# Optimization experiments

Hardware: AMD Instinct MI355X
Metric: run time of the kernel (lower is better)

The kernel has to match this reference:

```python
import jax, jax.numpy as jnp
import numpy as np

N0, N1, N2 = 200000, 50000, 10000   # node counts per hop (src -> layer1 targets -> layer2 targets)
E1, E2 = 1000000, 250000
C_IN, H = 128, 256


def setup_inputs() -> dict:
    key = jax.random.key(0)
    ks = jax.random.split(key, 10)
    return {
        "x": jax.random.normal(ks[0], (N0, C_IN), dtype=jnp.float32),
        "src1": jax.random.randint(ks[1], (E1,), 0, N0, dtype=jnp.int32),
        "dst1": jax.random.randint(ks[2], (E1,), 0, N1, dtype=jnp.int32),
        "src2": jax.random.randint(ks[3], (E2,), 0, N1, dtype=jnp.int32),
        "dst2": jax.random.randint(ks[4], (E2,), 0, N2, dtype=jnp.int32),
        "Wl1": jax.random.normal(ks[5], (C_IN, H), dtype=jnp.float32) / np.sqrt(C_IN),
        "Wr1": jax.random.normal(ks[6], (C_IN, H), dtype=jnp.float32) / np.sqrt(C_IN),
        "b1": jnp.zeros((H,), dtype=jnp.float32),
        "Wl2": jax.random.normal(ks[7], (H, H), dtype=jnp.float32) / np.sqrt(H),
        "Wr2": jax.random.normal(ks[8], (H, H), dtype=jnp.float32) / np.sqrt(H),
        "b2": jnp.zeros((H,), dtype=jnp.float32),
    }


def _sage_conv(x_src, x_dst, src, dst, Wl, Wr, b, n_dst):
    # mean aggregation of neighbor messages (PyG SAGEConv, aggr='mean', root_weight=True)
    msgs = x_src[src]                                             # [E, C] irregular gather
    agg = jax.ops.segment_sum(msgs, dst, num_segments=n_dst)      # [n_dst, C]
    cnt = jax.ops.segment_sum(jnp.ones_like(dst, dtype=x_src.dtype), dst, num_segments=n_dst)
    agg = agg / jnp.maximum(cnt, 1.0)[:, None]
    return agg @ Wl + x_dst @ Wr + b


def reference(x, src1, dst1, src2, dst2, Wl1, Wr1, b1, Wl2, Wr2, b2):
    # layer 1: targets are first N1 nodes
    h = _sage_conv(x, x[:N1], src1, dst1, Wl1, Wr1, b1, N1)       # [N1, H]
    h = jax.nn.relu(h)                                            # dropout: eval mode (identity)
    # layer 2: targets are first N2 nodes of the layer-1 output
    out = _sage_conv(h, h[:N2], src2, dst2, Wl2, Wr2, b2, N2)     # [N2, H]
    return out
```

## Files before the change

### kernel.cpp

```cpp
#include <hip/hip_runtime.h>

#define N0 200000
#define N1 50000
#define N2 10000
#define E1 1000000
#define E2 250000
#define CIN 128
#define HD  256

#define SH1   7
#define PK1   18
#define NB1   391
#define CAP1  3072
#define DPB1  128
#define SH2   6
#define PK2   16
#define NB2   157
#define CAP2  2048
#define DPB2  64

#define NBIN1 489
#define NBIN2 123
#define NPREP 768
#define NCVT  25000

typedef __attribute__((ext_vector_type(8))) short short8;
typedef __attribute__((ext_vector_type(4))) float f32x4;

__device__ __forceinline__ unsigned short f2bf(float f) {
    unsigned u = __builtin_bit_cast(unsigned, f);
    u = (u + 0x7fffu + ((u >> 16) & 1u)) >> 16;
    return (unsigned short)u;
}
__device__ __forceinline__ float bf2f(unsigned short h) {
    unsigned u = ((unsigned)h) << 16;
    return __builtin_bit_cast(float, u);
}

template<int SHIFTB, int PACKSH, int CAP>
__device__ __forceinline__ void bin_body(
    int bb, const int* __restrict__ src, const int* __restrict__ dst,
    int* __restrict__ gcnt, unsigned* __restrict__ binned, int E, int* sh)
{
    int* hcnt  = sh;
    int* hbase = sh + 512;
    int* hcur  = sh + 1024;
    const int t = threadIdx.x;
    hcnt[t] = 0; hcnt[t + 256] = 0;
    __syncthreads();

    unsigned pk[8];
    int      bk[8];
    const int e0 = bb * 2048;
    #pragma unroll
    for (int j = 0; j < 8; j++) {
        const int e = e0 + j * 256 + t;
        if (e < E) {
            const int d = dst[e];
            const int s = src[e];
            bk[j] = d >> SHIFTB;
            pk[j] = ((unsigned)(d & ((1 << SHIFTB) - 1)) << PACKSH) | (unsigned)s;
            atomicAdd(&hcnt[bk[j]], 1);
        } else bk[j] = -1;
    }
    __syncthreads();

    hbase[t]       = atomicAdd(&gcnt[t], hcnt[t]);             hcur[t] = 0;
    hbase[t + 256] = atomicAdd(&gcnt[t + 256], hcnt[t + 256]); hcur[t + 256] = 0;
    __syncthreads();

    #pragma unroll
    for (int j = 0; j < 8; j++) {
        if (bk[j] >= 0) {
            const int idx = atomicAdd(&hcur[bk[j]], 1);
            binned[(size_t)bk[j] * CAP + hbase[bk[j]] + idx] = pk[j];
        }
    }
}

__global__ __launch_bounds__(256) void megaA_kernel(
    const float* __restrict__ x, unsigned short* __restrict__ xb,
    const float* __restrict__ Wl1, const float* __restrict__ Wr1,
    const float* __restrict__ Wl2, const float* __restrict__ Wr2,
    unsigned short* __restrict__ wsw1, unsigned short* __restrict__ wsw2,
    const int* __restrict__ src1, const int* __restrict__ dst1,
    const int* __restrict__ src2, const int* __restrict__ dst2,
    int* __restrict__ gcnt1, int* __restrict__ gcnt2,
    unsigned* __restrict__ binned1, unsigned* __restrict__ binned2)
{
    __shared__ int sh[1536];
    const int b = blockIdx.x;
    const int t = threadIdx.x;

    if (b < NBIN1) {
        bin_body<SH1, PK1, CAP1>(b, src1, dst1, gcnt1, binned1, E1, sh);
    } else if (b < NBIN1 + NBIN2) {
        bin_body<SH2, PK2, CAP2>(b - NBIN1, src2, dst2, gcnt2, binned2, E2, sh);
    } else if (b < NBIN1 + NBIN2 + NPREP) {
        const int pb = b - NBIN1 - NBIN2;
        const float* Wl; const float* Wr; unsigned short* wsw; int K, tid;
        if (pb < 256) { Wl = Wl1; Wr = Wr1; wsw = wsw1; K = CIN; tid = pb * 256 + t; }
        else          { Wl = Wl2; Wr = Wr2; wsw = wsw2; K = HD;  tid = (pb - 256) * 256 + t; }
        const int j  = tid & 7;
        const int L  = (tid >> 3) & 63;
        const int nt = (tid >> 9) & 15;
        const int kt = tid >> 13;
        const int k  = kt * 32 + (L >> 4) * 8 + j;
        const int n  = nt * 16 + (L & 15);
        const float v = (k < K) ? Wl[(size_t)k * HD + n]
                                : Wr[(size_t)(k - K) * HD + n];
        wsw[tid] = f2bf(v);
    } else {
        const int i = (b - NBIN1 - NBIN2 - NPREP) * 256 + t;
        const float4 v = ((const float4*)x)[i];
        ushort4 o;
        o.x = f2bf(v.x); o.y = f2bf(v.y); o.z = f2bf(v.z); o.w = f2bf(v.w);
        ((ushort4*)xb)[i] = o;
    }
}

__global__ __launch_bounds__(512) void layer1_mega(
    const unsigned short* __restrict__ xb,
    const unsigned* __restrict__ binned1, const int* __restrict__ gcnt1,
    const unsigned short* __restrict__ wsw1, const float* __restrict__ bias,
    unsigned short* __restrict__ hb)
{
    __shared__ int ebuf[CAP1];
    __shared__ int lhist[DPB1], loff[DPB1], lcur[DPB1];
    __shared__ __align__(16) unsigned short aggT[4 * 128 * 4 * 8];

    const int t = threadIdx.x;
    const int b = blockIdx.x;
    const int cnt = gcnt1[b];
    const unsigned* bp = binned1 + (size_t)b * CAP1;

    if (t < DPB1) lhist[t] = 0;
    __syncthreads();
    for (int i = t; i < cnt; i += 512)
        atomicAdd(&lhist[bp[i] >> PK1], 1);
    __syncthreads();
    const int h0 = (t < DPB1) ? lhist[t] : 0;
    __syncthreads();
    #pragma unroll
    for (int ofs = 1; ofs < DPB1; ofs <<= 1) {
        const int u = (t >= ofs && t < DPB1) ? lhist[t - ofs] : 0;
        __syncthreads();
        if (t < DPB1) lhist[t] += u;
        __syncthreads();
    }
    if (t < DPB1) { loff[t] = lhist[t] - h0; lcur[t] = lhist[t] - h0; }
    __syncthreads();
    for (int i = t; i < cnt; i += 512) {
        const unsigned p = bp[i];
        const int slot = atomicAdd(&lcur[p >> PK1], 1);
        ebuf[slot] = (int)(p & ((1u << PK1) - 1u));
    }
    __syncthreads();

    const int w = t >> 6, L = t & 63, half = L >> 5, l32 = L & 31;
    const int ktw = l32 >> 3, qw = (l32 >> 1) & 3, jo = (l32 & 1) * 4;
    for (int r = w; r < DPB1; r += 8) {
        const int rg = b * DPB1 + r;
        if (rg < N1) {
            const int base = loff[r];
            const int n    = lcur[r] - loff[r];
            float ax = 0.f, ay = 0.f, az = 0.f, aw = 0.f;
            int i = half;
            for (; i + 6 < n; i += 8) {
                const int s0 = ebuf[base + i];
                const int s1 = ebuf[base + i + 2];
                const int s2 = ebuf[base + i + 4];
                const int s3 = ebuf[base + i + 6];
                const ushort4 v0 = *(const ushort4*)(xb + (size_t)s0 * CIN + l32 * 4);
                const ushort4 v1 = *(const ushort4*)(xb + (size_t)s1 * CIN + l32 * 4);
                const ushort4 v2 = *(const ushort4*)(xb + (size_t)s2 * CIN + l32 * 4);
                const ushort4 v3 = *(const ushort4*)(xb + (size_t)s3 * CIN + l32 * 4);
                ax += bf2f(v0.x) + bf2f(v1.x) + bf2f(v2.x) + bf2f(v3.x);
                ay += bf2f(v0.y) + bf2f(v1.y) + bf2f(v2.y) + bf2f(v3.y);
                az += bf2f(v0.z) + bf2f(v1.z) + bf2f(v2.z) + bf2f(v3.z);
                aw += bf2f(v0.w) + bf2f(v1.w) + bf2f(v2.w) + bf2f(v3.w);
            }
            for (; i < n; i += 2) {
                const int s = ebuf[base + i];
                const ushort4 v = *(const ushort4*)(xb + (size_t)s * CIN + l32 * 4);
                ax += bf2f(v.x); ay += bf2f(v.y); az += bf2f(v.z); aw += bf2f(v.w);
            }
            ax += __shfl_xor(ax, 32);
            ay += __shfl_xor(ay, 32);
            az += __shfl_xor(az, 32);
            aw += __shfl_xor(aw, 32);
            if (half == 0) {
                const float s = 1.0f / fmaxf((float)n, 1.0f);
                ushort4 o;
                o.x = f2bf(ax * s); o.y = f2bf(ay * s);
                o.z = f2bf(az * s); o.w = f2bf(aw * s);
                *(ushort4*)&aggT[(((ktw * 128 + r) * 4 + qw) * 8) + jo] = o;
            }
        }
    }
    __syncthreads();

    const int m = L & 15, q = L >> 4;
    const int row_l = w * 16 + m;
    const int rg2 = min(b * DPB1 + row_l, N1 - 1);
    const unsigned short* a2p = xb + (size_t)rg2 * CIN + q * 8;

    f32x4 acc[16];
    #pragma unroll
    for (int nt = 0; nt < 16; nt++) acc[nt] = (f32x4){0.f, 0.f, 0.f, 0.f};

    #pragma unroll
    for (int kt = 0; kt < 8; kt++) {
        short8 af;
        if (kt < 4) af = *(const short8*)&aggT[((kt * 128 + row_l) * 4 + q) * 8];
        else        af = *(const short8*)(a2p + (kt - 4) * 32);
        #pragma unroll
        for (int nt = 0; nt < 16; nt++) {
            const short8 bf = *(const short8*)(
                wsw1 + (((size_t)kt * 16 + nt) * 64 + L) * 8);
            acc[nt] = __builtin_amdgcn_mfma_f32_16x16x32_bf16(af, bf, acc[nt], 0, 0, 0);
        }
    }

    const int orow0 = b * DPB1 + w * 16 + q * 4;
    #pragma unroll
    for (int nt = 0; nt < 16; nt++) {
        const int col = nt * 16 + m;
        const float bv = bias[col];
        #pragma unroll
        for (int r = 0; r < 4; r++) {
            const int row = orow0 + r;
            if (row < N1) {
                const float v = fmaxf(acc[nt][r] + bv, 0.0f);
                hb[(size_t)row * HD + col] = f2bf(v);
            }
        }
    }
}

__global__ __launch_bounds__(512) void layer2_mega(
    const unsigned short* __restrict__ hb,
    const unsigned* __restrict__ binned2, const int* __restrict__ gcnt2,
    const unsigned short* __restrict__ wsw2, const float* __restrict__ bias,
    float* __restrict__ outp)
{
    __shared__ int ebuf[CAP2];
    __shared__ int lhist[DPB2], loff[DPB2], lcur[DPB2];
    __shared__ __align__(16) unsigned short aggT[8 * 64 * 4 * 8];

    const int t = threadIdx.x;
    const int b = blockIdx.x;
    const int cnt = gcnt2[b];
    const unsigned* bp = binned2 + (size_t)b * CAP2;

    if (t < DPB2) lhist[t] = 0;
    __syncthreads();
    for (int i = t; i < cnt; i += 512)
        atomicAdd(&lhist[bp[i] >> PK2], 1);
    __syncthreads();
    const int h0 = (t < DPB2) ? lhist[t] : 0;
    __syncthreads();
    #pragma unroll
    for (int ofs = 1; ofs < DPB2; ofs <<= 1) {
        const int u = (t >= ofs && t < DPB2) ? lhist[t - ofs] : 0;
        __syncthreads();
        if (t < DPB2) lhist[t] += u;
        __syncthreads();
    }
    if (t < DPB2) { loff[t] = lhist[t] - h0; lcur[t] = lhist[t] - h0; }
    __syncthreads();
    for (int i = t; i < cnt; i += 512) {
        const unsigned p = bp[i];
        const int slot = atomicAdd(&lcur[p >> PK2], 1);
        ebuf[slot] = (int)(p & ((1u << PK2) - 1u));
    }
    __syncthreads();

    const int w = t >> 6, L = t & 63;
    const int kt2 = L >> 3, q2 = (L >> 1) & 3, jo2 = (L & 1) * 4;
    for (int r = w; r < DPB2; r += 8) {
        const int rg = b * DPB2 + r;
        if (rg < N2) {
            const int base = loff[r];
            const int n    = lcur[r] - loff[r];
            float ax = 0.f, ay = 0.f, az = 0.f, aw = 0.f;
            int i = 0;
            for (; i + 3 < n; i += 4) {
                const int s0 = ebuf[base + i];
                const int s1 = ebuf[base + i + 1];
                const int s2 = ebuf[base + i + 2];
                const int s3 = ebuf[base + i + 3];
                const ushort4 v0 = *(const ushort4*)(hb + (size_t)s0 * HD + L * 4);
                const ushort4 v1 = *(const ushort4*)(hb + (size_t)s1 * HD + L * 4);
                const ushort4 v2 = *(const ushort4*)(hb + (size_t)s2 * HD + L * 4);
                const ushort4 v3 = *(const ushort4*)(hb + (size_t)s3 * HD + L * 4);
                ax += bf2f(v0.x) + bf2f(v1.x) + bf2f(v2.x) + bf2f(v3.x);
                ay += bf2f(v0.y) + bf2f(v1.y) + bf2f(v2.y) + bf2f(v3.y);
                az += bf2f(v0.z) + bf2f(v1.z) + bf2f(v2.z) + bf2f(v3.z);
                aw += bf2f(v0.w) + bf2f(v1.w) + bf2f(v2.w) + bf2f(v3.w);
            }
            for (; i < n; i++) {
                const int s = ebuf[base + i];
                const ushort4 v = *(const ushort4*)(hb + (size_t)s * HD + L * 4);
                ax += bf2f(v.x); ay += bf2f(v.y); az += bf2f(v.z); aw += bf2f(v.w);
            }
            const float s = 1.0f / fmaxf((float)n, 1.0f);
            ushort4 o;
            o.x = f2bf(ax * s); o.y = f2bf(ay * s);
            o.z = f2bf(az * s); o.w = f2bf(aw * s);
            *(ushort4*)&aggT[(((kt2 * 64 + r) * 4 + q2) * 8) + jo2] = o;
        }
    }
    __syncthreads();

    const int m = L & 15, q = L >> 4;
    const int mt = w & 3, nh = w >> 2;
    const int row_l = mt * 16 + m;
    const int rg2 = min(b * DPB2 + row_l, N2 - 1);
    const unsigned short* a2p = hb + (size_t)rg2 * HD + q * 8;

    f32x4 acc[8];
    #pragma unroll
    for (int nt = 0; nt < 8; nt++) acc[nt] = (f32x4){0.f, 0.f, 0.f, 0.f};

    #pragma unroll
    for (int kt = 0; kt < 16; kt++) {
        short8 af;
        if (kt < 8) af = *(const short8*)&aggT[((kt * 64 + row_l) * 4 + q) * 8];
        else        af = *(const short8*)(a2p + (kt - 8) * 32);
        #pragma unroll
        for (int nt = 0; nt < 8; nt++) {
            const short8 bf = *(const short8*)(
                wsw2 + (((size_t)kt * 16 + (nh * 8 + nt)) * 64 + L) * 8);
            acc[nt] = __builtin_amdgcn_mfma_f32_16x16x32_bf16(af, bf, acc[nt], 0, 0, 0);
        }
    }

    const int orow0 = b * DPB2 + mt * 16 + q * 4;
    #pragma unroll
    for (int nt = 0; nt < 8; nt++) {
        const int col = (nh * 8 + nt) * 16 + m;
        const float bv = bias[col];
        #pragma unroll
        for (int r = 0; r < 4; r++) {
            const int row = orow0 + r;
            if (row < N2)
                outp[(size_t)row * HD + col] = acc[nt][r] + bv;
        }
    }
}

extern "C" void kernel_launch(void* const* d_in, const int* in_sizes, int n_in,
                              void* d_out, int out_size, void* d_ws, size_t ws_size,
                              hipStream_t stream)
{
    const float* x    = (const float*)d_in[0];
    const int*   src1 = (const int*)  d_in[1];
    const int*   dst1 = (const int*)  d_in[2];
    const int*   src2 = (const int*)  d_in[3];
    const int*   dst2 = (const int*)  d_in[4];
    const float* Wl1  = (const float*)d_in[5];
    const float* Wr1  = (const float*)d_in[6];
    const float* b1   = (const float*)d_in[7];
    const float* Wl2  = (const float*)d_in[8];
    const float* Wr2  = (const float*)d_in[9];
    const float* b2   = (const float*)d_in[10];
    float* out = (float*)d_out;

    unsigned short* xb   = (unsigned short*)d_ws;
    unsigned short* hb   = xb + (size_t)N0 * CIN;
    unsigned short* wsw1 = hb + (size_t)N1 * HD;
    unsigned short* wsw2 = wsw1 + 2 * CIN * HD;
    int* gcnt1 = (int*)(wsw2 + 2 * HD * HD);
    int* gcnt2 = gcnt1 + 512;
    unsigned* binned1 = (unsigned*)(gcnt2 + 512);
    unsigned* binned2 = binned1 + (size_t)NB1 * CAP1;

    hipMemsetAsync(gcnt1, 0, 1024 * sizeof(int), stream);

    megaA_kernel<<<NBIN1 + NBIN2 + NPREP + NCVT, 256, 0, stream>>>(
        x, xb, Wl1, Wr1, Wl2, Wr2, wsw1, wsw2,
        src1, dst1, src2, dst2, gcnt1, gcnt2, binned1, binned2);

    layer1_mega<<<NB1, 512, 0, stream>>>(xb, binned1, gcnt1, wsw1, b1, hb);
    layer2_mega<<<NB2, 512, 0, stream>>>(hb, binned2, gcnt2, wsw2, b2, out);
}
```

Before: 310.2 us.

## Shrink destination bins to double layer1 and quadruple layer2 block counts

Halves the destinations per block in layer 1 (128 to 64) and cuts layer 2 from 64 to 16, so the launches have 782 and 625 blocks instead of 391 and 157 and can fill more compute units. The binning histograms grow to 1024 buckets, and the MFMA output tiling is re-split across warps so each warp covers fewer columns. The gather loops are also unrolled to issue 8 independent loads before accumulating, to hide more memory latency. The smaller per-bin capacities (2048 and 640 edges) leave less headroom for skewed degree distributions, and each block now reloads its full weight slice, which adds weight traffic.

Result: no change. 306.8 us (-1.1%).

```diff
diff --git a/kernel.cpp b/kernel.cpp
--- a/kernel.cpp
+++ b/kernel.cpp
@@ -8,16 +8,16 @@
 #define CIN 128
 #define HD  256
 
-#define SH1   7
+#define SH1   6
 #define PK1   18
-#define NB1   391
-#define CAP1  3072
-#define DPB1  128
-#define SH2   6
+#define NB1   782
+#define CAP1  2048
+#define DPB1  64
+#define SH2   4
 #define PK2   16
-#define NB2   157
-#define CAP2  2048
-#define DPB2  64
+#define NB2   625
+#define CAP2  640
+#define DPB2  16
 
 #define NBIN1 489
 #define NBIN2 123
@@ -43,10 +43,11 @@
     int* __restrict__ gcnt, unsigned* __restrict__ binned, int E, int* sh)
 {
     int* hcnt  = sh;
-    int* hbase = sh + 512;
-    int* hcur  = sh + 1024;
+    int* hbase = sh + 1024;
+    int* hcur  = sh + 2048;
     const int t = threadIdx.x;
-    hcnt[t] = 0; hcnt[t + 256] = 0;
+    #pragma unroll
+    for (int j = 0; j < 4; j++) hcnt[t + j * 256] = 0;
     __syncthreads();
 
     unsigned pk[8];
@@ -65,8 +66,12 @@
     }
     __syncthreads();
 
-    hbase[t]       = atomicAdd(&gcnt[t], hcnt[t]);             hcur[t] = 0;
-    hbase[t + 256] = atomicAdd(&gcnt[t + 256], hcnt[t + 256]); hcur[t + 256] = 0;
+    #pragma unroll
+    for (int j = 0; j < 4; j++) {
+        const int i = t + j * 256;
+        hbase[i] = atomicAdd(&gcnt[i], hcnt[i]);
+        hcur[i]  = 0;
+    }
     __syncthreads();
 
     #pragma unroll
@@ -88,7 +93,7 @@
     int* __restrict__ gcnt1, int* __restrict__ gcnt2,
     unsigned* __restrict__ binned1, unsigned* __restrict__ binned2)
 {
-    __shared__ int sh[1536];
+    __shared__ int sh[3072];
     const int b = blockIdx.x;
     const int t = threadIdx.x;
 
@@ -127,7 +132,7 @@
 {
     __shared__ int ebuf[CAP1];
     __shared__ int lhist[DPB1], loff[DPB1], lcur[DPB1];
-    __shared__ __align__(16) unsigned short aggT[4 * 128 * 4 * 8];
+    __shared__ __align__(16) unsigned short aggT[4 * DPB1 * 4 * 8];
 
     const int t = threadIdx.x;
     const int b = blockIdx.x;
@@ -166,19 +171,18 @@
             const int n    = lcur[r] - loff[r];
             float ax = 0.f, ay = 0.f, az = 0.f, aw = 0.f;
             int i = half;
-            for (; i + 6 < n; i += 8) {
-                const int s0 = ebuf[base + i];
-                const int s1 = ebuf[base + i + 2];
-                const int s2 = ebuf[base + i + 4];
-                const int s3 = ebuf[base + i + 6];
-                const ushort4 v0 = *(const ushort4*)(xb + (size_t)s0 * CIN + l32 * 4);
-                const ushort4 v1 = *(const ushort4*)(xb + (size_t)s1 * CIN + l32 * 4);
-                const ushort4 v2 = *(const ushort4*)(xb + (size_t)s2 * CIN + l32 * 4);
-                const ushort4 v3 = *(const ushort4*)(xb + (size_t)s3 * CIN + l32 * 4);
-                ax += bf2f(v0.x) + bf2f(v1.x) + bf2f(v2.x) + bf2f(v3.x);
-                ay += bf2f(v0.y) + bf2f(v1.y) + bf2f(v2.y) + bf2f(v3.y);
-                az += bf2f(v0.z) + bf2f(v1.z) + bf2f(v2.z) + bf2f(v3.z);
-                aw += bf2f(v0.w) + bf2f(v1.w) + bf2f(v2.w) + bf2f(v3.w);
+            for (; i + 14 < n; i += 16) {
+                ushort4 v[8];
+                #pragma unroll
+                for (int u = 0; u < 8; u++) {
+                    const int s = ebuf[base + i + u * 2];
+                    v[u] = *(const ushort4*)(xb + (size_t)s * CIN + l32 * 4);
+                }
+                #pragma unroll
+                for (int u = 0; u < 8; u++) {
+                    ax += bf2f(v[u].x); ay += bf2f(v[u].y);
+                    az += bf2f(v[u].z); aw += bf2f(v[u].w);
+                }
             }
             for (; i < n; i += 2) {
                 const int s = ebuf[base + i];
@@ -194,38 +198,39 @@
                 ushort4 o;
                 o.x = f2bf(ax * s); o.y = f2bf(ay * s);
                 o.z = f2bf(az * s); o.w = f2bf(aw * s);
-                *(ushort4*)&aggT[(((ktw * 128 + r) * 4 + qw) * 8) + jo] = o;
+                *(ushort4*)&aggT[(((ktw * DPB1 + r) * 4 + qw) * 8) + jo] = o;
             }
         }
     }
     __syncthreads();
 
     const int m = L & 15, q = L >> 4;
-    const int row_l = w * 16 + m;
+    const int mt = w & 3, nh = w >> 2;
+    const int row_l = mt * 16 + m;
     const int rg2 = min(b * DPB1 + row_l, N1 - 1);
     const unsigned short* a2p = xb + (size_t)rg2 * CIN + q * 8;
 
-    f32x4 acc[16];
-    #pragma unroll
-    for (int nt = 0; nt < 16; nt++) acc[nt] = (f32x4){0.f, 0.f, 0.f, 0.f};
+    f32x4 acc[8];
+    #pragma unroll
+    for (int nt = 0; nt < 8; nt++) acc[nt] = (f32x4){0.f, 0.f, 0.f, 0.f};
 
     #pragma unroll
     for (int kt = 0; kt < 8; kt++) {
         short8 af;
-        if (kt < 4) af = *(const short8*)&aggT[((kt * 128 + row_l) * 4 + q) * 8];
+        if (kt < 4) af = *(const short8*)&aggT[((kt * DPB1 + row_l) * 4 + q) * 8];
         else        af = *(const short8*)(a2p + (kt - 4) * 32);
         #pragma unroll
-        for (int nt = 0; nt < 16; nt++) {
+        for (int nt = 0; nt < 8; nt++) {
             const short8 bf = *(const short8*)(
-                wsw1 + (((size_t)kt * 16 + nt) * 64 + L) * 8);
+                wsw1 + (((size_t)kt * 16 + (nh * 8 + nt)) * 64 + L) * 8);
             acc[nt] = __builtin_amdgcn_mfma_f32_16x16x32_bf16(af, bf, acc[nt], 0, 0, 0);
         }
     }
 
-    const int orow0 = b * DPB1 + w * 16 + q * 4;
-    #pragma unroll
-    for (int nt = 0; nt < 16; nt++) {
-        const int col = nt * 16 + m;
+    const int orow0 = b * DPB1 + mt * 16 + q * 4;
+    #pragma unroll
+    for (int nt = 0; nt < 8; nt++) {
+        const int col = (nh * 8 + nt) * 16 + m;
         const float bv = bias[col];
         #pragma unroll
         for (int r = 0; r < 4; r++) {
@@ -246,7 +251,7 @@
 {
     __shared__ int ebuf[CAP2];
     __shared__ int lhist[DPB2], loff[DPB2], lcur[DPB2];
-    __shared__ __align__(16) unsigned short aggT[8 * 64 * 4 * 8];
+    __shared__ __align__(16) unsigned short aggT[8 * DPB2 * 4 * 8];
 
     const int t = threadIdx.x;
     const int b = blockIdx.x;
@@ -279,74 +284,65 @@
     const int w = t >> 6, L = t & 63;
     const int kt2 = L >> 3, q2 = (L >> 1) & 3, jo2 = (L & 1) * 4;
     for (int r = w; r < DPB2; r += 8) {
-        const int rg = b * DPB2 + r;
-        if (rg < N2) {
-            const int base = loff[r];
-            const int n    = lcur[r] - loff[r];
-            float ax = 0.f, ay = 0.f, az = 0.f, aw = 0.f;
-            int i = 0;
-            for (; i + 3 < n; i += 4) {
-                const int s0 = ebuf[base + i];
-                const int s1 = ebuf[base + i + 1];
-                const int s2 = ebuf[base + i + 2];
-                const int s3 = ebuf[base + i + 3];
-                const ushort4 v0 = *(const ushort4*)(hb + (size_t)s0 * HD + L * 4);
-                const ushort4 v1 = *(const ushort4*)(hb + (size_t)s1 * HD + L * 4);
-                const ushort4 v2 = *(const ushort4*)(hb + (size_t)s2 * HD + L * 4);
-                const ushort4 v3 = *(const ushort4*)(hb + (size_t)s3 * HD + L * 4);
-                ax += bf2f(v0.x) + bf2f(v1.x) + bf2f(v2.x) + bf2f(v3.x);
-                ay += bf2f(v0.y) + bf2f(v1.y) + bf2f(v2.y) + bf2f(v3.y);
-                az += bf2f(v0.z) + bf2f(v1.z) + bf2f(v2.z) + bf2f(v3.z);
-                aw += bf2f(v0.w) + bf2f(v1.w) + bf2f(v2.w) + bf2f(v3.w);
-            }
-            for (; i < n; i++) {
-                const int s = ebuf[base + i];
-                const ushort4 v = *(const ushort4*)(hb + (size_t)s * HD + L * 4);
-                ax += bf2f(v.x); ay += bf2f(v.y); az += bf2f(v.z); aw += bf2f(v.w);
-            }
-            const float s = 1.0f / fmaxf((float)n, 1.0f);
-            ushort4 o;
-            o.x = f2bf(ax * s); o.y = f2bf(ay * s);
-            o.z = f2bf(az * s); o.w = f2bf(aw * s);
-            *(ushort4*)&aggT[(((kt2 * 64 + r) * 4 + q2) * 8) + jo2] = o;
-        }
+        const int base = loff[r];
+        const int n    = lcur[r] - loff[r];
+        float ax = 0.f, ay = 0.f, az = 0.f, aw = 0.f;
+        int i = 0;
+        for (; i + 7 < n; i += 8) {
+            ushort4 v[8];
+            #pragma unroll
+            for (int u = 0; u < 8; u++) {
+                const int s = ebuf[base + i + u];
+                v[u] = *(const ushort4*)(hb + (size_t)s * HD + L * 4);
+            }
+            #pragma unroll
+            for (int u = 0; u < 8; u++) {
+                ax += bf2f(v[u].x); ay += bf2f(v[u].y);
+                az += bf2f(v[u].z); aw += bf2f(v[u].w);
+            }
+        }
+        for (; i < n; i++) {
+            const int s = ebuf[base + i];
+            const ushort4 v = *(const ushort4*)(hb + (size_t)s * HD + L * 4);
+            ax += bf2f(v.x); ay += bf2f(v.y); az += bf2f(v.z); aw += bf2f(v.w);
+        }
+        const float s = 1.0f / fmaxf((float)n, 1.0f);
+        ushort4 o;
+        o.x = f2bf(ax * s); o.y = f2bf(ay * s);
+        o.z = f2bf(az * s); o.w = f2bf(aw * s);
+        *(ushort4*)&aggT[(((kt2 * DPB2 + r) * 4 + q2) * 8) + jo2] = o;
     }
     __syncthreads();
 
     const int m = L & 15, q = L >> 4;
-    const int mt = w & 3, nh = w >> 2;
-    const int row_l = mt * 16 + m;
-    const int rg2 = min(b * DPB2 + row_l, N2 - 1);
+    const int rg2 = b * DPB2 + m;
     const unsigned short* a2p = hb + (size_t)rg2 * HD + q * 8;
 
-    f32x4 acc[8];
-    #pragma unroll
-    for (int nt = 0; nt < 8; nt++) acc[nt] = (f32x4){0.f, 0.f, 0.f, 0.f};
+    f32x4 acc[2];
+    acc[0] = (f32x4){0.f, 0.f, 0.f, 0.f};
+    acc[1] = (f32x4){0.f, 0.f, 0.f, 0.f};
 
     #pragma unroll
     for (int kt = 0; kt < 16; kt++) {
         short8 af;
-        if (kt < 8) af = *(const short8*)&aggT[((kt * 64 + row_l) * 4 + q) * 8];
+        if (kt < 8) af = *(const short8*)&aggT[((kt * DPB2 + m) * 4 + q) * 8];
         else        af = *(const short8*)(a2p + (kt - 8) * 32);
         #pragma unroll
-        for (int nt = 0; nt < 8; nt++) {
+        for (int nt = 0; nt < 2; nt++) {
             const short8 bf = *(const short8*)(
-                wsw2 + (((size_t)kt * 16 + (nh * 8 + nt)) * 64 + L) * 8);
+                wsw2 + (((size_t)kt * 16 + (w * 2 + nt)) * 64 + L) * 8);
             acc[nt] = __builtin_amdgcn_mfma_f32_16x16x32_bf16(af, bf, acc[nt], 0, 0, 0);
         }
     }
 
-    const int orow0 = b * DPB2 + mt * 16 + q * 4;
-    #pragma unroll
-    for (int nt = 0; nt < 8; nt++) {
-        const int col = (nh * 8 + nt) * 16 + m;
+    const int orow0 = b * DPB2 + q * 4;
+    #pragma unroll
+    for (int nt = 0; nt < 2; nt++) {
+        const int col = (w * 2 + nt) * 16 + m;
         const float bv = bias[col];
         #pragma unroll
-        for (int r = 0; r < 4; r++) {
-            const int row = orow0 + r;
-            if (row < N2)
-                outp[(size_t)row * HD + col] = acc[nt][r] + bv;
-        }
+        for (int r = 0; r < 4; r++)
+            outp[(size_t)(orow0 + r) * HD + col] = acc[nt][r] + bv;
     }
 }
 
@@ -372,11 +368,11 @@
     unsigned short* wsw1 = hb + (size_t)N1 * HD;
     unsigned short* wsw2 = wsw1 + 2 * CIN * HD;
     int* gcnt1 = (int*)(wsw2 + 2 * HD * HD);
-    int* gcnt2 = gcnt1 + 512;
-    unsigned* binned1 = (unsigned*)(gcnt2 + 512);
+    int* gcnt2 = gcnt1 + 1024;
+    unsigned* binned1 = (unsigned*)(gcnt2 + 1024);
     unsigned* binned2 = binned1 + (size_t)NB1 * CAP1;
 
-    hipMemsetAsync(gcnt1, 0, 1024 * sizeof(int), stream);
+    hipMemsetAsync(gcnt1, 0, 2048 * sizeof(int), stream);
 
     megaA_kernel<<<NBIN1 + NBIN2 + NPREP + NCVT, 256, 0, stream>>>(
         x, xb, Wl1, Wr1, Wl2, Wr2, wsw1, wsw2,
```
